# Kernel optimization log

Hardware: AMD Instinct MI355X
Metric: run time of the kernel (lower is better)

The kernel has to match this reference:

```python
import jax, jax.numpy as jnp
import numpy as np

LN_EPS = 1e-5


def _layer_norm(x, w, b, eps=LN_EPS):
    mu = jnp.mean(x, axis=-1, keepdims=True)
    var = jnp.var(x, axis=-1, keepdims=True)
    return (x - mu) * jax.lax.rsqrt(var + eps) * w + b


def setup_inputs() -> dict:
    key = jax.random.key(0)
    ks = jax.random.split(key, 6)
    H, I, B, S = 1024, 4096, 4, 2048
    return {
        "x": jax.random.normal(ks[0], (B, S, H), jnp.float32),
        "ln_weight": jnp.ones((H,), jnp.float32),
        "ln_bias": jnp.zeros((H,), jnp.float32),
        "i2h_weight": jax.random.normal(ks[1], (2 * I, H), jnp.float32) * 0.02,
        "i2h_bias": jax.random.normal(ks[2], (2 * I,), jnp.float32) * 0.02,
        "h2o_weight": jax.random.normal(ks[3], (H, I), jnp.float32) * 0.02,
        "h2o_bias": jax.random.normal(ks[4], (H,), jnp.float32) * 0.02,
        "post_ln_weight": jnp.ones((H,), jnp.float32),
        "post_ln_bias": jnp.zeros((H,), jnp.float32),
    }


def reference(x, ln_weight, ln_bias, i2h_weight, i2h_bias, h2o_weight, h2o_bias,
              post_ln_weight, post_ln_bias):
    B, S, H = x.shape
    x2 = x.reshape(-1, H)  # [N, H]
    x_ln = _layer_norm(x2, ln_weight, ln_bias)
    # i2h: [N, 2I]
    pre = jnp.einsum('nh,oh->no', x_ln, i2h_weight) + i2h_bias
    I = pre.shape[-1] // 2
    pre_gate, lin = pre[:, :I], pre[:, I:]
    # gated gelu (tanh-approx, matching gelu_fused)
    hid = jax.nn.gelu(pre_gate, approximate=True) * lin
    out = jnp.einsum('ni,oi->no', hid, h2o_weight) + h2o_bias
    out = _layer_norm(out, post_ln_weight, post_ln_bias)
    out = out + x2  # residual (dropout=0)
    return out.reshape(B, S, H)
```

## Files before the change

kernel.cpp:

```cpp
#include <hip/hip_runtime.h>
#include <stdint.h>

#define N_ROWS 8192
#define H_DIM  1024
#define I_DIM  4096

typedef unsigned short u16;
typedef __bf16 bf16x8 __attribute__((ext_vector_type(8)));
typedef float f32x4 __attribute__((ext_vector_type(4)));
typedef u16 u16x4 __attribute__((ext_vector_type(4)));

#define BAR()   asm volatile("s_barrier" ::: "memory")
#define VMW(n)  asm volatile("s_waitcnt vmcnt(" #n ")" ::: "memory")

__device__ __forceinline__ u16 f2bf(float f) {
    union { float f; uint32_t u; } v; v.f = f;
    uint32_t u = v.u;
    u += 0x7FFFu + ((u >> 16) & 1u);
    return (u16)(u >> 16);
}

__device__ __forceinline__ float bf2f(u16 h) {
    union { uint32_t u; float f; } v; v.u = ((uint32_t)h) << 16;
    return v.f;
}

__device__ __forceinline__ float gelu_tanh(float x) {
    float u = 0.7978845608028654f * (x + 0.044715f * x * x * x);
    u = fminf(fmaxf(u, -15.f), 15.f);
    float e = __expf(2.f * u);
    float t = (e - 1.f) / (e + 1.f);
    return 0.5f * x * (1.f + t);
}

__device__ __forceinline__ void load_lds16(const void* g, void* l) {
    auto gp = reinterpret_cast<const __attribute__((address_space(1))) uint32_t*>(
        reinterpret_cast<uintptr_t>(g));
    auto lp = reinterpret_cast<__attribute__((address_space(3))) uint32_t*>(
        static_cast<uint32_t>(reinterpret_cast<uintptr_t>(l)));
    __builtin_amdgcn_global_load_lds(gp, lp, 16, 0, 0);
}

__global__ __launch_bounds__(512, 4) void gemm1_gated(
    const u16* __restrict__ A, const u16* __restrict__ W,
    const float* __restrict__ bias, u16* __restrict__ hid)
{
    __shared__ u16 lds[3 * 12288];
    const int t = threadIdx.x;
    const int lane = t & 63, wid = t >> 6;
    const int wm = wid >> 2, wn = wid & 3;
    const int g = lane >> 4, r16 = lane & 15;

    const int brow = blockIdx.y * 128;
    const int bcol = blockIdx.x * 128;

    const int tr = t >> 2;
    const int swz8 = ((t & 3) ^ ((tr >> 1) & 3)) * 8;
    const u16* pA  = A + (size_t)(brow + tr) * H_DIM + swz8;
    const u16* pBg = W + (size_t)(bcol + tr) * H_DIM + swz8;
    const u16* pBl = W + (size_t)(I_DIM + bcol + tr) * H_DIM + swz8;
    const int dst = t * 8;

    const int sl  = (g ^ ((r16 >> 1) & 3)) * 8;
    const int rdA = (wm * 64 + r16) * 32 + sl;
    const int rdB = 4096 + (wn * 32 + r16) * 32 + sl;

    f32x4 accg[4][2] = {};
    f32x4 accl[4][2] = {};

#define STG1(S, k0) do { \
    load_lds16(pA  + (k0), (S) + dst); \
    load_lds16(pBg + (k0), (S) + 4096 + dst); \
    load_lds16(pBl + (k0), (S) + 8192 + dst); } while (0)

    STG1(lds, 0);
    STG1(lds + 12288, 32);
    VMW(3); BAR();

    const int NT = H_DIM / 32;
    int bc = 0;
#pragma unroll 1
    for (int kt = 0; kt < NT; ++kt) {
        const u16* L = lds + bc * 12288;
        if (kt + 2 < NT) {
            u16* S = lds + ((bc + 2 >= 3) ? (bc - 1) : (bc + 2)) * 12288;
            STG1(S, (kt + 2) * 32);
        }
        bf16x8 af[4], bg[2], bl[2];
#pragma unroll
        for (int m = 0; m < 4; ++m) af[m] = *(const bf16x8*)(L + rdA + m * 512);
#pragma unroll
        for (int n = 0; n < 2; ++n) {
            bg[n] = *(const bf16x8*)(L + rdB + n * 512);
            bl[n] = *(const bf16x8*)(L + rdB + 4096 + n * 512);
        }
        __builtin_amdgcn_s_setprio(1);
#pragma unroll
        for (int m = 0; m < 4; ++m)
#pragma unroll
            for (int n = 0; n < 2; ++n) {
                accg[m][n] = __builtin_amdgcn_mfma_f32_16x16x32_bf16(af[m], bg[n], accg[m][n], 0, 0, 0);
                accl[m][n] = __builtin_amdgcn_mfma_f32_16x16x32_bf16(af[m], bl[n], accl[m][n], 0, 0, 0);
            }
        __builtin_amdgcn_s_setprio(0);
        if (kt + 2 < NT) { VMW(3); } else { VMW(0); }
        BAR();
        bc = (bc == 2) ? 0 : bc + 1;
    }
#undef STG1

#pragma unroll
    for (int n = 0; n < 2; ++n) {
        const int cg = bcol + wn * 32 + n * 16 + r16;
        const float bgv = bias[cg], blv = bias[I_DIM + cg];
#pragma unroll
        for (int m = 0; m < 4; ++m) {
            const int row = brow + wm * 64 + m * 16 + g * 4;
            u16* hp = hid + (size_t)row * I_DIM + cg;
#pragma unroll
            for (int r = 0; r < 4; ++r) {
                float gate = accg[m][n][r] + bgv;
                float lin  = accl[m][n][r] + blv;
                hp[(size_t)r * I_DIM] = f2bf(gelu_tanh(gate) * lin);
            }
        }
    }
}

__global__ __launch_bounds__(256, 3) void gemm2_k(
    const u16* __restrict__ A, const u16* __restrict__ W,
    const float* __restrict__ bias, u16* __restrict__ opb)
{
    __shared__ u16 lds[3 * 8192];
    const int t = threadIdx.x;
    const int lane = t & 63, wid = t >> 6;
    const int wm = wid >> 1, wn = wid & 1;
    const int g = lane >> 4, r16 = lane & 15;

    const int brow = blockIdx.y * 128;
    const int bcol = blockIdx.x * 128;

    const int tr = t >> 2;
    const int swz8 = ((t & 3) ^ ((tr >> 1) & 3)) * 8;
    const u16* pA = A + (size_t)(brow + tr) * I_DIM + swz8;
    const u16* pB = W + (size_t)(bcol + tr) * I_DIM + swz8;
    const int dst = t * 8;

    const int sl  = (g ^ ((r16 >> 1) & 3)) * 8;
    const int rdA = (wm * 64 + r16) * 32 + sl;
    const int rdB = 4096 + (wn * 64 + r16) * 32 + sl;

    f32x4 acc[4][4] = {};

#define STG2(S, k0) do { \
    load_lds16(pA + (k0),                      (S) + dst); \
    load_lds16(pA + (size_t)64 * I_DIM + (k0), (S) + 2048 + dst); \
    load_lds16(pB + (k0),                      (S) + 4096 + dst); \
    load_lds16(pB + (size_t)64 * I_DIM + (k0), (S) + 6144 + dst); } while (0)

    STG2(lds, 0);
    STG2(lds + 8192, 32);
    VMW(4); BAR();

    const int NT = I_DIM / 32;
    int bc = 0;
#pragma unroll 1
    for (int kt = 0; kt < NT; ++kt) {
        const u16* L = lds + bc * 8192;
        if (kt + 2 < NT) {
            u16* S = lds + ((bc + 2 >= 3) ? (bc - 1) : (bc + 2)) * 8192;
            STG2(S, (kt + 2) * 32);
        }
        bf16x8 af[4], bf[4];
#pragma unroll
        for (int m = 0; m < 4; ++m) af[m] = *(const bf16x8*)(L + rdA + m * 512);
#pragma unroll
        for (int n = 0; n < 4; ++n) bf[n] = *(const bf16x8*)(L + rdB + n * 512);
        __builtin_amdgcn_s_setprio(1);
#pragma unroll
        for (int m = 0; m < 4; ++m)
#pragma unroll
            for (int n = 0; n < 4; ++n)
                acc[m][n] = __builtin_amdgcn_mfma_f32_16x16x32_bf16(af[m], bf[n], acc[m][n], 0, 0, 0);
        __builtin_amdgcn_s_setprio(0);
        if (kt + 2 < NT) { VMW(4); } else { VMW(0); }
        BAR();
        bc = (bc == 2) ? 0 : bc + 1;
    }
#undef STG2

#pragma unroll
    for (int n = 0; n < 4; ++n) {
        const int cg = bcol + wn * 64 + n * 16 + r16;
        const float bv = bias[cg];
#pragma unroll
        for (int m = 0; m < 4; ++m) {
            const int row = brow + wm * 64 + m * 16 + g * 4;
            u16* op = opb + (size_t)row * H_DIM + cg;
#pragma unroll
            for (int r = 0; r < 4; ++r)
                op[(size_t)r * H_DIM] = f2bf(acc[m][n][r] + bv);
        }
    }
}

__device__ __forceinline__ void block_mean_var(float s, float s2, float* red, int t,
                                               float& mu, float& var) {
#pragma unroll
    for (int off = 32; off > 0; off >>= 1) {
        s  += __shfl_down(s, off);
        s2 += __shfl_down(s2, off);
    }
    const int wid = t >> 6;
    if ((t & 63) == 0) { red[wid] = s; red[4 + wid] = s2; }
    __syncthreads();
    if (t == 0) {
        float a = red[0] + red[1] + red[2] + red[3];
        float b = red[4] + red[5] + red[6] + red[7];
        red[0] = a * (1.f / H_DIM);
        red[1] = b * (1.f / H_DIM);
    }
    __syncthreads();
    mu = red[0];
    var = red[1] - mu * mu;
}

__global__ __launch_bounds__(256) void prep(
    const float* __restrict__ x, const float* __restrict__ lnw,
    const float* __restrict__ lnb, u16* __restrict__ xln,
    const float* __restrict__ w1, u16* __restrict__ w1b,
    const float* __restrict__ w2, u16* __restrict__ w2b)
{
    __shared__ float red[8];
    const int bid = blockIdx.x, t = threadIdx.x;
    if (bid < N_ROWS) {
        const float4 v = reinterpret_cast<const float4*>(x + (size_t)bid * H_DIM)[t];
        float mu, var;
        block_mean_var(v.x + v.y + v.z + v.w,
                       v.x * v.x + v.y * v.y + v.z * v.z + v.w * v.w, red, t, mu, var);
        const float rstd = rsqrtf(var + 1e-5f);
        const float4 wv = reinterpret_cast<const float4*>(lnw)[t];
        const float4 bv = reinterpret_cast<const float4*>(lnb)[t];
        u16x4 o;
        o.x = f2bf((v.x - mu) * rstd * wv.x + bv.x);
        o.y = f2bf((v.y - mu) * rstd * wv.y + bv.y);
        o.z = f2bf((v.z - mu) * rstd * wv.z + bv.z);
        o.w = f2bf((v.w - mu) * rstd * wv.w + bv.w);
        reinterpret_cast<u16x4*>(xln + (size_t)bid * H_DIM)[t] = o;
    } else if (bid < N_ROWS + 8192) {
        const int i = (bid - N_ROWS) * 256 + t;
        const float4 v = reinterpret_cast<const float4*>(w1)[i];
        u16x4 o = { f2bf(v.x), f2bf(v.y), f2bf(v.z), f2bf(v.w) };
        reinterpret_cast<u16x4*>(w1b)[i] = o;
    } else {
        const int i = (bid - N_ROWS - 8192) * 256 + t;
        const float4 v = reinterpret_cast<const float4*>(w2)[i];
        u16x4 o = { f2bf(v.x), f2bf(v.y), f2bf(v.z), f2bf(v.w) };
        reinterpret_cast<u16x4*>(w2b)[i] = o;
    }
}

__global__ void ln_post_res(const u16* __restrict__ op, const float* __restrict__ w,
                            const float* __restrict__ b, const float* __restrict__ x,
                            float* __restrict__ out)
{
    __shared__ float red[8];
    const int row = blockIdx.x, t = threadIdx.x;
    const u16x4 hv = reinterpret_cast<const u16x4*>(op + (size_t)row * H_DIM)[t];
    float4 v;
    v.x = bf2f(hv.x); v.y = bf2f(hv.y); v.z = bf2f(hv.z); v.w = bf2f(hv.w);
    float mu, var;
    block_mean_var(v.x + v.y + v.z + v.w,
                   v.x * v.x + v.y * v.y + v.z * v.z + v.w * v.w, red, t, mu, var);
    const float rstd = rsqrtf(var + 1e-5f);
    const float4 wv = reinterpret_cast<const float4*>(w)[t];
    const float4 bv = reinterpret_cast<const float4*>(b)[t];
    const float4 xv = reinterpret_cast<const float4*>(x + (size_t)row * H_DIM)[t];
    float4 o;
    o.x = (v.x - mu) * rstd * wv.x + bv.x + xv.x;
    o.y = (v.y - mu) * rstd * wv.y + bv.y + xv.y;
    o.z = (v.z - mu) * rstd * wv.z + bv.z + xv.z;
    o.w = (v.w - mu) * rstd * wv.w + bv.w + xv.w;
    reinterpret_cast<float4*>(out + (size_t)row * H_DIM)[t] = o;
}

extern "C" void kernel_launch(void* const* d_in, const int* in_sizes, int n_in,
                              void* d_out, int out_size, void* d_ws, size_t ws_size,
                              hipStream_t stream)
{
    const float* x   = (const float*)d_in[0];
    const float* lnw = (const float*)d_in[1];
    const float* lnb = (const float*)d_in[2];
    const float* w1  = (const float*)d_in[3];
    const float* b1  = (const float*)d_in[4];
    const float* w2  = (const float*)d_in[5];
    const float* b2  = (const float*)d_in[6];
    const float* pw  = (const float*)d_in[7];
    const float* pb  = (const float*)d_in[8];
    float* out = (float*)d_out;

    char* ws = (char*)d_ws;
    u16* xln = (u16*)(ws);
    u16* w1b = (u16*)(ws + (16u << 20));
    u16* hid = (u16*)(ws + (32u << 20));
    u16* w2b = (u16*)(ws + (96u << 20));
    u16* opb = (u16*)(ws);

    prep<<<20480, 256, 0, stream>>>(x, lnw, lnb, xln, w1, w1b, w2, w2b);
    gemm1_gated<<<dim3(I_DIM / 128, N_ROWS / 128), 512, 0, stream>>>(xln, w1b, b1, hid);
    gemm2_k<<<dim3(H_DIM / 128, N_ROWS / 128), 256, 0, stream>>>(hid, w2b, b2, opb);
    ln_post_res<<<N_ROWS, 256, 0, stream>>>(opb, pw, pb, x, out);
}
```

Baseline: 272.0 us.

## Enlarge gemm1 tile to 256 rows with interleaved gate/linear B tile

```diff
diff --git a/kernel.cpp b/kernel.cpp
--- a/kernel.cpp
+++ b/kernel.cpp
@@ -41,69 +41,68 @@
     __builtin_amdgcn_global_load_lds(gp, lp, 16, 0, 0);
 }
 
-__global__ __launch_bounds__(512, 4) void gemm1_gated(
+__global__ __launch_bounds__(512, 2) void gemm1_gated(
     const u16* __restrict__ A, const u16* __restrict__ W,
     const float* __restrict__ bias, u16* __restrict__ hid)
 {
-    __shared__ u16 lds[3 * 12288];
+    __shared__ u16 lds[3 * 16384];
     const int t = threadIdx.x;
     const int lane = t & 63, wid = t >> 6;
     const int wm = wid >> 2, wn = wid & 3;
     const int g = lane >> 4, r16 = lane & 15;
 
-    const int brow = blockIdx.y * 128;
+    const int brow = blockIdx.y * 256;
     const int bcol = blockIdx.x * 128;
 
     const int tr = t >> 2;
     const int swz8 = ((t & 3) ^ ((tr >> 1) & 3)) * 8;
-    const u16* pA  = A + (size_t)(brow + tr) * H_DIM + swz8;
-    const u16* pBg = W + (size_t)(bcol + tr) * H_DIM + swz8;
-    const u16* pBl = W + (size_t)(I_DIM + bcol + tr) * H_DIM + swz8;
+    const u16* pA = A + (size_t)(brow + tr) * H_DIM + swz8;
+    const int j0 = tr, j1 = tr + 128;
+    const int c0 = bcol + ((j0 >> 6) << 5) + (j0 & 31);
+    const int c1 = bcol + ((j1 >> 6) << 5) + (j1 & 31);
+    const u16* pB0 = W + (size_t)(((j0 & 63) < 32) ? c0 : (I_DIM + c0)) * H_DIM + swz8;
+    const u16* pB1 = W + (size_t)(((j1 & 63) < 32) ? c1 : (I_DIM + c1)) * H_DIM + swz8;
     const int dst = t * 8;
 
     const int sl  = (g ^ ((r16 >> 1) & 3)) * 8;
-    const int rdA = (wm * 64 + r16) * 32 + sl;
-    const int rdB = 4096 + (wn * 32 + r16) * 32 + sl;
-
-    f32x4 accg[4][2] = {};
-    f32x4 accl[4][2] = {};
+    const int rdA = (wm * 128 + r16) * 32 + sl;
+    const int rdB = 8192 + (wn * 64 + r16) * 32 + sl;
+
+    f32x4 acc[8][4] = {};
 
 #define STG1(S, k0) do { \
-    load_lds16(pA  + (k0), (S) + dst); \
-    load_lds16(pBg + (k0), (S) + 4096 + dst); \
-    load_lds16(pBl + (k0), (S) + 8192 + dst); } while (0)
+    load_lds16(pA  + (k0),                       (S) + dst); \
+    load_lds16(pA  + (size_t)128 * H_DIM + (k0), (S) + 4096 + dst); \
+    load_lds16(pB0 + (k0),                       (S) + 8192 + dst); \
+    load_lds16(pB1 + (k0),                       (S) + 12288 + dst); } while (0)
 
     STG1(lds, 0);
-    STG1(lds + 12288, 32);
-    VMW(3); BAR();
+    STG1(lds + 16384, 32);
+    VMW(4); BAR();
 
     const int NT = H_DIM / 32;
     int bc = 0;
 #pragma unroll 1
     for (int kt = 0; kt < NT; ++kt) {
-        const u16* L = lds + bc * 12288;
-        if (kt + 2 < NT) {
-            u16* S = lds + ((bc + 2 >= 3) ? (bc - 1) : (bc + 2)) * 12288;
+        const u16* L = lds + bc * 16384;
+        const bool st = (kt + 2 < NT);
+        if (st) {
+            u16* S = lds + ((bc + 2 >= 3) ? (bc - 1) : (bc + 2)) * 16384;
             STG1(S, (kt + 2) * 32);
         }
-        bf16x8 af[4], bg[2], bl[2];
-#pragma unroll
-        for (int m = 0; m < 4; ++m) af[m] = *(const bf16x8*)(L + rdA + m * 512);
-#pragma unroll
-        for (int n = 0; n < 2; ++n) {
-            bg[n] = *(const bf16x8*)(L + rdB + n * 512);
-            bl[n] = *(const bf16x8*)(L + rdB + 4096 + n * 512);
-        }
+        bf16x8 af[8], bf[4];
+#pragma unroll
+        for (int m = 0; m < 8; ++m) af[m] = *(const bf16x8*)(L + rdA + m * 512);
+#pragma unroll
+        for (int n = 0; n < 4; ++n) bf[n] = *(const bf16x8*)(L + rdB + n * 512);
         __builtin_amdgcn_s_setprio(1);
 #pragma unroll
-        for (int m = 0; m < 4; ++m)
-#pragma unroll
-            for (int n = 0; n < 2; ++n) {
-                accg[m][n] = __builtin_amdgcn_mfma_f32_16x16x32_bf16(af[m], bg[n], accg[m][n], 0, 0, 0);
-                accl[m][n] = __builtin_amdgcn_mfma_f32_16x16x32_bf16(af[m], bl[n], accl[m][n], 0, 0, 0);
-            }
+        for (int m = 0; m < 8; ++m)
+#pragma unroll
+            for (int n = 0; n < 4; ++n)
+                acc[m][n] = __builtin_amdgcn_mfma_f32_16x16x32_bf16(af[m], bf[n], acc[m][n], 0, 0, 0);
         __builtin_amdgcn_s_setprio(0);
-        if (kt + 2 < NT) { VMW(3); } else { VMW(0); }
+        if (st) { VMW(4); } else { VMW(0); }
         BAR();
         bc = (bc == 2) ? 0 : bc + 1;
     }
@@ -114,13 +113,13 @@
         const int cg = bcol + wn * 32 + n * 16 + r16;
         const float bgv = bias[cg], blv = bias[I_DIM + cg];
 #pragma unroll
-        for (int m = 0; m < 4; ++m) {
-            const int row = brow + wm * 64 + m * 16 + g * 4;
+        for (int m = 0; m < 8; ++m) {
+            const int row = brow + wm * 128 + m * 16 + g * 4;
             u16* hp = hid + (size_t)row * I_DIM + cg;
 #pragma unroll
             for (int r = 0; r < 4; ++r) {
-                float gate = accg[m][n][r] + bgv;
-                float lin  = accl[m][n][r] + blv;
+                float gate = acc[m][n][r] + bgv;
+                float lin  = acc[m][n + 2][r] + blv;
                 hp[(size_t)r * I_DIM] = f2bf(gelu_tanh(gate) * lin);
             }
         }
@@ -307,7 +306,7 @@
     u16* opb = (u16*)(ws);
 
     prep<<<20480, 256, 0, stream>>>(x, lnw, lnb, xln, w1, w1b, w2, w2b);
-    gemm1_gated<<<dim3(I_DIM / 128, N_ROWS / 128), 512, 0, stream>>>(xln, w1b, b1, hid);
+    gemm1_gated<<<dim3(I_DIM / 128, N_ROWS / 256), 512, 0, stream>>>(xln, w1b, b1, hid);
     gemm2_k<<<dim3(H_DIM / 128, N_ROWS / 128), 256, 0, stream>>>(hid, w2b, b2, opb);
     ln_post_res<<<N_ROWS, 256, 0, stream>>>(opb, pw, pb, x, out);
 }
```

After: 274.9 us. About the same (+1.1%).

## Enlarge gemm2 tile to 256x128 with 512 threads and double-buffered 64-wide K stages

Applied to the files above, without the earlier changes.

```diff
diff --git a/kernel.cpp b/kernel.cpp
--- a/kernel.cpp
+++ b/kernel.cpp
@@ -11,6 +11,7 @@
 typedef u16 u16x4 __attribute__((ext_vector_type(4)));
 
 #define BAR()   asm volatile("s_barrier" ::: "memory")
+#define LGKM0() asm volatile("s_waitcnt lgkmcnt(0)" ::: "memory")
 #define VMW(n)  asm volatile("s_waitcnt vmcnt(" #n ")" ::: "memory")
 
 __device__ __forceinline__ u16 f2bf(float f) {
@@ -127,17 +128,17 @@
     }
 }
 
-__global__ __launch_bounds__(256, 3) void gemm2_k(
+__global__ __launch_bounds__(512, 2) void gemm2_k(
     const u16* __restrict__ A, const u16* __restrict__ W,
     const float* __restrict__ bias, u16* __restrict__ opb)
 {
-    __shared__ u16 lds[3 * 8192];
+    __shared__ u16 lds[2 * 24576];
     const int t = threadIdx.x;
     const int lane = t & 63, wid = t >> 6;
     const int wm = wid >> 1, wn = wid & 1;
     const int g = lane >> 4, r16 = lane & 15;
 
-    const int brow = blockIdx.y * 128;
+    const int brow = blockIdx.y * 256;
     const int bcol = blockIdx.x * 128;
 
     const int tr = t >> 2;
@@ -148,46 +149,72 @@
 
     const int sl  = (g ^ ((r16 >> 1) & 3)) * 8;
     const int rdA = (wm * 64 + r16) * 32 + sl;
-    const int rdB = 4096 + (wn * 64 + r16) * 32 + sl;
+    const int rdB = 16384 + (wn * 64 + r16) * 32 + sl;
 
     f32x4 acc[4][4] = {};
 
-#define STG2(S, k0) do { \
-    load_lds16(pA + (k0),                      (S) + dst); \
-    load_lds16(pA + (size_t)64 * I_DIM + (k0), (S) + 2048 + dst); \
-    load_lds16(pB + (k0),                      (S) + 4096 + dst); \
-    load_lds16(pB + (size_t)64 * I_DIM + (k0), (S) + 6144 + dst); } while (0)
-
-    STG2(lds, 0);
-    STG2(lds + 8192, 32);
-    VMW(4); BAR();
-
-    const int NT = I_DIM / 32;
-    int bc = 0;
+    u16* const B0 = lds;
+    u16* const B1 = lds + 24576;
+
+#define STG_A2(S, kk, ks) do { \
+    load_lds16(pA + (kk) + (ks) * 32,                       (S) + (ks) * 8192 + dst); \
+    load_lds16(pA + (size_t)128 * I_DIM + (kk) + (ks) * 32, (S) + (ks) * 8192 + 4096 + dst); } while (0)
+#define STG_B2(S, kk, ks) do { \
+    load_lds16(pB + (kk) + (ks) * 32, (S) + 16384 + (ks) * 4096 + dst); } while (0)
+#define RD2(L, ks) { _Pragma("unroll") for (int m = 0; m < 4; ++m) \
+    af[m] = *(const bf16x8*)((L) + (ks) * 8192 + rdA + m * 512); \
+    _Pragma("unroll") for (int n = 0; n < 4; ++n) \
+    bf[n] = *(const bf16x8*)((L) + (ks) * 4096 + rdB + n * 512); }
+#define MM2() { _Pragma("unroll") for (int m = 0; m < 4; ++m) _Pragma("unroll") for (int n = 0; n < 4; ++n) \
+    acc[m][n] = __builtin_amdgcn_mfma_f32_16x16x32_bf16(af[m], bf[n], acc[m][n], 0, 0, 0); }
+
+    STG_A2(B0, 0, 0); STG_B2(B0, 0, 0);
+    STG_A2(B0, 0, 1); STG_B2(B0, 0, 1);
+    STG_A2(B1, 64, 0); STG_B2(B1, 64, 0);
+    VMW(6); BAR();
+
+    const int NI = I_DIM / 128;
 #pragma unroll 1
-    for (int kt = 0; kt < NT; ++kt) {
-        const u16* L = lds + bc * 8192;
-        if (kt + 2 < NT) {
-            u16* S = lds + ((bc + 2 >= 3) ? (bc - 1) : (bc + 2)) * 8192;
-            STG2(S, (kt + 2) * 32);
-        }
+    for (int it = 0; it < NI; ++it) {
+        const int kkO  = (2 * it + 1) * 64;
+        const int kkE2 = (2 * it + 2) * 64;
+        const int kkO2 = (2 * it + 3) * 64;
+        const bool s2 = (it + 1 < NI);
+        const bool last = (it == NI - 1);
         bf16x8 af[4], bf[4];
-#pragma unroll
-        for (int m = 0; m < 4; ++m) af[m] = *(const bf16x8*)(L + rdA + m * 512);
-#pragma unroll
-        for (int n = 0; n < 4; ++n) bf[n] = *(const bf16x8*)(L + rdB + n * 512);
-        __builtin_amdgcn_s_setprio(1);
-#pragma unroll
-        for (int m = 0; m < 4; ++m)
-#pragma unroll
-            for (int n = 0; n < 4; ++n)
-                acc[m][n] = __builtin_amdgcn_mfma_f32_16x16x32_bf16(af[m], bf[n], acc[m][n], 0, 0, 0);
-        __builtin_amdgcn_s_setprio(0);
-        if (kt + 2 < NT) { VMW(4); } else { VMW(0); }
-        BAR();
-        bc = (bc == 2) ? 0 : bc + 1;
-    }
-#undef STG2
+
+        STG_A2(B1, kkO, 1); STG_B2(B1, kkO, 1);
+        RD2(B0, 0);
+        BAR(); LGKM0();
+        __builtin_amdgcn_s_setprio(1); MM2(); __builtin_amdgcn_s_setprio(0);
+        VMW(6);
+        BAR();
+
+        if (s2) { STG_A2(B0, kkE2, 0); STG_B2(B0, kkE2, 0); }
+        RD2(B0, 1);
+        BAR(); LGKM0();
+        __builtin_amdgcn_s_setprio(1); MM2(); __builtin_amdgcn_s_setprio(0);
+        if (last) { VMW(3); } else { VMW(6); }
+        BAR();
+
+        if (s2) { STG_A2(B0, kkE2, 1); STG_B2(B0, kkE2, 1); }
+        RD2(B1, 0);
+        BAR(); LGKM0();
+        __builtin_amdgcn_s_setprio(1); MM2(); __builtin_amdgcn_s_setprio(0);
+        if (last) { VMW(0); } else { VMW(6); }
+        BAR();
+
+        if (s2) { STG_A2(B1, kkO2, 0); STG_B2(B1, kkO2, 0); }
+        RD2(B1, 1);
+        BAR(); LGKM0();
+        __builtin_amdgcn_s_setprio(1); MM2(); __builtin_amdgcn_s_setprio(0);
+        if (!last) { VMW(6); }
+        BAR();
+    }
+#undef STG_A2
+#undef STG_B2
+#undef RD2
+#undef MM2
 
 #pragma unroll
     for (int n = 0; n < 4; ++n) {
@@ -308,6 +335,6 @@
 
     prep<<<20480, 256, 0, stream>>>(x, lnw, lnb, xln, w1, w1b, w2, w2b);
     gemm1_gated<<<dim3(I_DIM / 128, N_ROWS / 128), 512, 0, stream>>>(xln, w1b, b1, hid);
-    gemm2_k<<<dim3(H_DIM / 128, N_ROWS / 128), 256, 0, stream>>>(hid, w2b, b2, opb);
+    gemm2_k<<<dim3(H_DIM / 128, N_ROWS / 256), 512, 0, stream>>>(hid, w2b, b2, opb);
     ln_post_res<<<N_ROWS, 256, 0, stream>>>(opb, pw, pb, x, out);
 }
```

Result: faster. 266.4 us (-2.0%).
